# Kernel optimization log

Measured on AMD Instinct MI355X. Metric: run time of the kernel, lower is better.

The kernel has to match this reference:

```python
import jax, jax.numpy as jnp
import numpy as np

N_ENTITIES = 100_000
N_USERS = 50_000
N_HOPS = 3
R0, R1 = 42033, 44630  # hard-coded region slice in the source (2597 regions)
CHANNEL = 128
N_EDGES = 2_000_000
NNZ = 1_000_000
N_REL_ROWS = 25  # n_relations - 1


def setup_inputs() -> dict:
    key = jax.random.key(0)
    ks = jax.random.split(key, 10)
    user_emb = jax.random.normal(ks[0], (N_USERS, CHANNEL), jnp.float32) * 0.1
    entity_emb = jax.random.normal(ks[1], (N_ENTITIES, CHANNEL), jnp.float32) * 0.1
    edge_head = jax.random.randint(ks[2], (N_EDGES,), 0, N_ENTITIES, dtype=jnp.int32)
    edge_tail = jax.random.randint(ks[3], (N_EDGES,), 0, N_ENTITIES, dtype=jnp.int32)
    # edge_type in [1, n_relations-1] because weight is indexed with edge_type - 1
    edge_type = jax.random.randint(ks[4], (N_EDGES,), 1, N_REL_ROWS + 1, dtype=jnp.int32)
    interact_rows = jax.random.randint(ks[5], (NNZ,), 0, N_USERS, dtype=jnp.int32)
    interact_cols = jax.random.randint(ks[6], (NNZ,), 0, N_ENTITIES, dtype=jnp.int32)
    interact_vals = jax.random.uniform(ks[7], (NNZ,), jnp.float32)
    rw = jax.random.uniform(ks[8], (R1 - R0, R1 - R0), jnp.float32)
    region_weight_matrix = rw / jnp.sum(rw, axis=1, keepdims=True)  # row-stochastic like source
    weight = jax.random.normal(ks[9], (N_REL_ROWS, CHANNEL), jnp.float32) * 0.1
    return {
        'user_emb': user_emb,
        'entity_emb': entity_emb,
        'region_weight_matrix': region_weight_matrix,
        'weight': weight,
        'interact_vals': interact_vals,
        'edge_head': edge_head,
        'edge_tail': edge_tail,
        'edge_type': edge_type,
        'interact_rows': interact_rows,
        'interact_cols': interact_cols,
    }


def _l2_normalize(x):
    # matches F.normalize(x, p=2, dim=1, eps=1e-12)
    n = jnp.linalg.norm(x, axis=1, keepdims=True)
    return x / jnp.maximum(n, 1e-12)


def reference(user_emb, entity_emb, region_weight_matrix, weight, interact_vals,
              edge_head, edge_tail, edge_type, interact_rows, interact_cols):
    entity_res, user_res = entity_emb, user_emb
    # scatter_mean denominator (edge structure is fixed across hops)
    deg = jax.ops.segment_sum(jnp.ones_like(edge_head, dtype=entity_emb.dtype),
                              edge_head, num_segments=N_ENTITIES)
    inv_deg = jnp.where(deg > 0, 1.0 / deg, 0.0)[:, None]

    for _ in range(N_HOPS):
        # region aggregate (source uses clone().detach())
        new_ev = jax.lax.stop_gradient(entity_emb)
        region = region_weight_matrix @ new_ev[R0:R1]  # [2597, C]
        new_ev = new_ev.at[R0:R1].set(region)
        entity_emb = entity_emb * 0.8 + new_ev * 0.2
        # KG aggregate: gather, relation-weighted multiply, scatter_mean by head
        rel = weight[edge_type - 1]                 # [E, C]
        neigh = entity_emb[edge_tail] * rel          # [E, C]
        entity_agg = jax.ops.segment_sum(neigh, edge_head, num_segments=N_ENTITIES) * inv_deg
        # user aggregate: sparse mm (COO) -> segment_sum over rows
        user_agg = jax.ops.segment_sum(interact_vals[:, None] * entity_emb[interact_cols],
                                       interact_rows, num_segments=N_USERS)
        # normalize + residual (mess_dropout disabled for deterministic reference)
        entity_emb = _l2_normalize(entity_agg)
        user_emb = _l2_normalize(user_agg)
        entity_res = entity_res + entity_emb
        user_res = user_res + user_emb
    return entity_res, user_res
```

## Files before the change

kernel.cpp:

```cpp
#include <hip/hip_runtime.h>
#include <stdint.h>

#define N_ENT 100000
#define N_USR 50000
#define NREG  2597
#define REG0  42033
#define CHAN  128
#define NEDGE 2000000
#define NNZI  1000000

#define BSPAN 512
#define NB_E  196
#define NB_U  98
#define BCAP  12288
#define TILE  2048
#define EPT   8
#define NWG_E ((NEDGE + TILE - 1) / TILE)
#define NWG_U ((NNZI  + TILE - 1) / TILE)

#define MT16   163
#define MPAD   (MT16 * 16)
#define KSTEPS 82
#define KPAD   (KSTEPS * 32)
#define NKC2   8
#define SPC    ((KSTEPS + NKC2 - 1) / NKC2)

typedef unsigned int uint32;
typedef unsigned short ushort16;
using bf16x8 = __attribute__((ext_vector_type(8))) short;
using f32x4  = __attribute__((ext_vector_type(4))) float;

__device__ __forceinline__ uint32 f2bf(float x) {
  uint32 b = __float_as_uint(x);
  b += 0x7FFFu + ((b >> 16) & 1u);
  return b >> 16;
}
__device__ __forceinline__ float bf_lo(uint32 u) { return __uint_as_float(u << 16); }
__device__ __forceinline__ float bf_hi(uint32 u) { return __uint_as_float(u & 0xFFFF0000u); }


__global__ __launch_bounds__(256) void k_part_e(const int* __restrict__ head,
                                                const int* __restrict__ tail,
                                                const int* __restrict__ type,
                                                int* __restrict__ cur,
                                                uint32* __restrict__ st) {
  __shared__ int lh[NB_E], lb[NB_E];
  int tid = threadIdx.x;
  for (int i = tid; i < NB_E; i += 256) lh[i] = 0;
  __syncthreads();
  int base = blockIdx.x * TILE;
  int bk[EPT], rk[EPT]; uint32 rec[EPT];
#pragma unroll
  for (int j = 0; j < EPT; ++j) {
    int idx = base + j * 256 + tid;
    bk[j] = -1;
    if (idx < NEDGE) {
      int h = head[idx];
      uint32 loc = (uint32)(h & (BSPAN - 1));
      rec[j] = (uint32)tail[idx] | ((uint32)(type[idx] - 1) << 17) | (loc << 22);
      bk[j] = h >> 9;
      rk[j] = atomicAdd(&lh[bk[j]], 1);
    }
  }
  __syncthreads();
  for (int i = tid; i < NB_E; i += 256)
    lb[i] = lh[i] ? atomicAdd(&cur[i], lh[i]) : 0;
  __syncthreads();
#pragma unroll
  for (int j = 0; j < EPT; ++j) {
    if (bk[j] >= 0) {
      int slot = lb[bk[j]] + rk[j];
      if (slot < BCAP) st[(size_t)bk[j] * BCAP + slot] = rec[j];
    }
  }
}

__global__ __launch_bounds__(256) void k_part_u(const int* __restrict__ rows,
                                                const int* __restrict__ cols,
                                                const float* __restrict__ vals,
                                                int* __restrict__ cur,
                                                uint2* __restrict__ st) {
  __shared__ int lh[NB_U], lb[NB_U];
  int tid = threadIdx.x;
  for (int i = tid; i < NB_U; i += 256) lh[i] = 0;
  __syncthreads();
  int base = blockIdx.x * TILE;
  int bk[EPT], rk[EPT]; uint2 rec[EPT];
#pragma unroll
  for (int j = 0; j < EPT; ++j) {
    int idx = base + j * 256 + tid;
    bk[j] = -1;
    if (idx < NNZI) {
      int r = rows[idx];
      uint32 loc = (uint32)(r & (BSPAN - 1));
      rec[j] = make_uint2(__float_as_uint(vals[idx]), (uint32)cols[idx] | (loc << 17));
      bk[j] = r >> 9;
      rk[j] = atomicAdd(&lh[bk[j]], 1);
    }
  }
  __syncthreads();
  for (int i = tid; i < NB_U; i += 256)
    lb[i] = lh[i] ? atomicAdd(&cur[i], lh[i]) : 0;
  __syncthreads();
#pragma unroll
  for (int j = 0; j < EPT; ++j) {
    if (bk[j] >= 0) {
      int slot = lb[bk[j]] + rk[j];
      if (slot < BCAP) st[(size_t)bk[j] * BCAP + slot] = rec[j];
    }
  }
}

__global__ void k_bexc(const int* __restrict__ cnt, int* __restrict__ base, int nb) {
  __shared__ int t[256];
  int tid = threadIdx.x;
  int x = (tid < nb) ? cnt[tid] : 0;
  t[tid] = x;
  __syncthreads();
  for (int off = 1; off < 256; off <<= 1) {
    int y = (tid >= off) ? t[tid - off] : 0;
    __syncthreads();
    t[tid] += y;
    __syncthreads();
  }
  if (tid < nb) base[tid] = t[tid] - x;
}

__global__ __launch_bounds__(512) void k_place_e(const uint32* __restrict__ st,
                                                 const int* __restrict__ bcnt,
                                                 const int* __restrict__ bbase,
                                                 int* __restrict__ rowptr,
                                                 float* __restrict__ invdeg,
                                                 int* __restrict__ pk) {
  __shared__ int hcnt[BSPAN];
  __shared__ int sx[BSPAN];
  int tid = threadIdx.x;
  int b = blockIdx.x;
  int cnt = bcnt[b]; if (cnt > BCAP) cnt = BCAP;
  int base = bbase[b];
  int h0 = b << 9;
  hcnt[tid] = 0;
  __syncthreads();
  const uint32* bst = st + (size_t)b * BCAP;
  for (int i = tid; i < cnt; i += 512)
    atomicAdd(&hcnt[(bst[i] >> 22) & (BSPAN - 1)], 1);
  __syncthreads();
  int mycnt = hcnt[tid];
  sx[tid] = mycnt;
  __syncthreads();
  for (int off = 1; off < 512; off <<= 1) {
    int y = (tid >= off) ? sx[tid - off] : 0;
    __syncthreads();
    sx[tid] += y;
    __syncthreads();
  }
  int myex = sx[tid] - mycnt;
  int gh = h0 + tid;
  if (gh <= N_ENT) rowptr[gh] = base + myex;
  if (gh < N_ENT) invdeg[gh] = mycnt ? 1.0f / (float)mycnt : 0.0f;
  __syncthreads();
  sx[tid] = base + myex;
  hcnt[tid] = 0;
  __syncthreads();
  for (int i = tid; i < cnt; i += 512) {
    uint32 r = bst[i];
    int loc = (r >> 22) & (BSPAN - 1);
    int rk = atomicAdd(&hcnt[loc], 1);
    pk[sx[loc] + rk] = (int)(r & 0x3FFFFFu);
  }
}

__global__ __launch_bounds__(512) void k_place_u(const uint2* __restrict__ st,
                                                 const int* __restrict__ bcnt,
                                                 const int* __restrict__ bbase,
                                                 int* __restrict__ rowptr,
                                                 int2* __restrict__ pk) {
  __shared__ int hcnt[BSPAN];
  __shared__ int sx[BSPAN];
  int tid = threadIdx.x;
  int b = blockIdx.x;
  int cnt = bcnt[b]; if (cnt > BCAP) cnt = BCAP;
  int base = bbase[b];
  int h0 = b << 9;
  hcnt[tid] = 0;
  __syncthreads();
  const uint2* bst = st + (size_t)b * BCAP;
  for (int i = tid; i < cnt; i += 512)
    atomicAdd(&hcnt[bst[i].y >> 17], 1);
  __syncthreads();
  int mycnt = hcnt[tid];
  sx[tid] = mycnt;
  __syncthreads();
  for (int off = 1; off < 512; off <<= 1) {
    int y = (tid >= off) ? sx[tid - off] : 0;
    __syncthreads();
    sx[tid] += y;
    __syncthreads();
  }
  int myex = sx[tid] - mycnt;
  int gh = h0 + tid;
  if (gh <= N_USR) rowptr[gh] = base + myex;
  __syncthreads();
  sx[tid] = base + myex;
  hcnt[tid] = 0;
  __syncthreads();
  for (int i = tid; i < cnt; i += 512) {
    uint2 r = bst[i];
    int loc = r.y >> 17;
    int rk = atomicAdd(&hcnt[loc], 1);
    pk[sx[loc] + rk] = make_int2((int)(r.y & 0x1FFFFu), (int)r.x);
  }
}

__global__ void k_cast_bf16(const float* __restrict__ src, uint32* __restrict__ dst, int n4) {
  int i = blockIdx.x * blockDim.x + threadIdx.x;
  if (i < n4) {
    float4 v = *(const float4*)(src + (size_t)i * 4);
    uint32 lo = f2bf(v.x) | (f2bf(v.y) << 16);
    uint32 hi = f2bf(v.z) | (f2bf(v.w) << 16);
    *(uint2*)(dst + (size_t)i * 2) = make_uint2(lo, hi);
  }
}

__global__ void k_cast_rwb(const float* __restrict__ RW, uint32* __restrict__ RWb) {
  int i = blockIdx.x * blockDim.x + threadIdx.x;
  if (i >= MPAD * (KPAD / 8)) return;
  int r = i / (KPAD / 8);
  int k0 = (i % (KPAD / 8)) * 8;
  uint32 o[4];
  if (r < NREG) {
    const float* s = RW + (size_t)r * NREG;
#pragma unroll
    for (int j = 0; j < 4; ++j) {
      int ka = k0 + 2 * j, kb = ka + 1;
      float va = (ka < NREG) ? s[ka] : 0.f;
      float vb = (kb < NREG) ? s[kb] : 0.f;
      o[j] = f2bf(va) | (f2bf(vb) << 16);
    }
  } else {
    o[0] = o[1] = o[2] = o[3] = 0u;
  }
  *(uint4*)(RWb + (size_t)r * (KPAD / 2) + k0 / 2) = make_uint4(o[0], o[1], o[2], o[3]);
}

__global__ void k_build_rbt(const float* __restrict__ Rf, uint32* __restrict__ RbT) {
  int i = blockIdx.x * blockDim.x + threadIdx.x;
  if (i >= CHAN * (KPAD / 8)) return;
  int c = i / (KPAD / 8);
  int k0 = (i % (KPAD / 8)) * 8;
  uint32 o[4];
#pragma unroll
  for (int j = 0; j < 4; ++j) {
    int ka = k0 + 2 * j, kb = ka + 1;
    float va = (ka < NREG) ? Rf[(size_t)ka * CHAN + c] : 0.f;
    float vb = (kb < NREG) ? Rf[(size_t)kb * CHAN + c] : 0.f;
    o[j] = f2bf(va) | (f2bf(vb) << 16);
  }
  *(uint4*)(RbT + (size_t)c * (KPAD / 2) + k0 / 2) = make_uint4(o[0], o[1], o[2], o[3]);
}

__global__ __launch_bounds__(256) void k_region_mfma(const ushort16* __restrict__ RWb,
                                                     const ushort16* __restrict__ RbT,
                                                     float* __restrict__ Rtmp) {
  int lane = threadIdx.x & 63;
  int wid  = threadIdx.x >> 6;
  int mt = blockIdx.x % MT16;
  int kc = blockIdx.x / MT16;
  int m0 = mt * 16;
  int rc  = lane & 15;
  int kq  = lane >> 4;

  int s0 = kc * SPC;
  int s1 = s0 + SPC; if (s1 > KSTEPS) s1 = KSTEPS;

  f32x4 acc0 = {0.f, 0.f, 0.f, 0.f};
  f32x4 acc1 = {0.f, 0.f, 0.f, 0.f};

  const ushort16* arow = RWb + (size_t)(m0 + rc) * KPAD;
  const ushort16* b0   = RbT + (size_t)(wid * 32 + rc) * KPAD;
  const ushort16* b1   = b0 + (size_t)16 * KPAD;

  for (int s = s0; s < s1; ++s) {
    int k = s * 32 + kq * 8;
    bf16x8 a  = *(const bf16x8*)(arow + k);
    bf16x8 v0 = *(const bf16x8*)(b0 + k);
    bf16x8 v1 = *(const bf16x8*)(b1 + k);
    acc0 = __builtin_amdgcn_mfma_f32_16x16x32_bf16(a, v0, acc0, 0, 0, 0);
    acc1 = __builtin_amdgcn_mfma_f32_16x16x32_bf16(a, v1, acc1, 0, 0, 0);
  }

  int orow = m0 + kq * 4;
#pragma unroll
  for (int r = 0; r < 4; ++r) {
    int gr = orow + r;
    if (gr < NREG) {
      atomicAdd(&Rtmp[(size_t)gr * CHAN + wid * 32 + rc],      acc0[r]);
      atomicAdd(&Rtmp[(size_t)gr * CHAN + wid * 32 + 16 + rc], acc1[r]);
    }
  }
}

__global__ void k_region_apply(float* __restrict__ Rf, const float* __restrict__ Rtmp,
                               ushort16* __restrict__ curB) {
  int i = blockIdx.x * blockDim.x + threadIdx.x;
  if (i < NREG * CHAN) {
    float v = Rf[i] * 0.8f + Rtmp[i] * 0.2f;
    Rf[i] = v;
    curB[(size_t)REG0 * CHAN + i] = (ushort16)f2bf(v);
  }
}


__global__ void k_ent_agg(const ushort16* __restrict__ curB, const int* __restrict__ rowptr,
                          const int* __restrict__ pk, const float* __restrict__ Wt,
                          const float* __restrict__ invdeg,
                          uint32* __restrict__ nxtB, float* __restrict__ nxtRf,
                          float* __restrict__ out_e) {
  int gid  = blockIdx.x * blockDim.x + threadIdx.x;
  int wave = gid >> 6;
  int lane = threadIdx.x & 63;
  if (wave >= N_ENT) return;
  int h = wave;
  int beg = rowptr[h], end = rowptr[h + 1];
  int deg = end - beg;
  int e = lane >> 4;
  int q = lane & 15;

  float acc[8];
#pragma unroll
  for (int k = 0; k < 8; ++k) acc[k] = 0.f;

  int pkv = 0;
  { int idx = beg + lane; if (idx < end) pkv = pk[idx]; }

  int nch = (deg + 3) >> 2;

  uint4  evA = make_uint4(0, 0, 0, 0);
  float4 waA = make_float4(0.f, 0.f, 0.f, 0.f);
  float4 wbA = make_float4(0.f, 0.f, 0.f, 0.f);
  uint32 mA = 0;

  if (nch > 0) {
    int p = __shfl(pkv, e, 64);
    mA = (e < deg) ? 0xFFFFFFFFu : 0u;
    int t = p & 0x1FFFF;
    int r = p >> 17;
    evA = *(const uint4*)((const char*)curB + ((size_t)t << 8) + (q << 4));
    const float* wr = Wt + ((size_t)r << 7) + (q << 3);
    waA = *(const float4*)wr;
    wbA = *(const float4*)(wr + 4);
  }

  for (int ci = 0; ci < nch; ++ci) {
    uint4  evB = make_uint4(0, 0, 0, 0);
    float4 waB = make_float4(0.f, 0.f, 0.f, 0.f);
    float4 wbB = make_float4(0.f, 0.f, 0.f, 0.f);
    uint32 mB = 0;
    int cn = ci + 1;
    if (cn < nch) {
      if ((cn & 15) == 0) {
        int idx = beg + cn * 4 + lane;
        pkv = (idx < end) ? pk[idx] : 0;
      }
      int p = __shfl(pkv, (cn & 15) * 4 + e, 64);
      mB = (cn * 4 + e < deg) ? 0xFFFFFFFFu : 0u;
      int t = p & 0x1FFFF;
      int r = p >> 17;
      evB = *(const uint4*)((const char*)curB + ((size_t)t << 8) + (q << 4));
      const float* wr = Wt + ((size_t)r << 7) + (q << 3);
      waB = *(const float4*)wr;
      wbB = *(const float4*)(wr + 4);
    }
    uint4 ev = evA;
    ev.x &= mA; ev.y &= mA; ev.z &= mA; ev.w &= mA;
    acc[0] += bf_lo(ev.x) * waA.x;
    acc[1] += bf_hi(ev.x) * waA.y;
    acc[2] += bf_lo(ev.y) * waA.z;
    acc[3] += bf_hi(ev.y) * waA.w;
    acc[4] += bf_lo(ev.z) * wbA.x;
    acc[5] += bf_hi(ev.z) * wbA.y;
    acc[6] += bf_lo(ev.w) * wbA.z;
    acc[7] += bf_hi(ev.w) * wbA.w;
    evA = evB; waA = waB; wbA = wbB; mA = mB;
  }

#pragma unroll
  for (int k = 0; k < 8; ++k) {
    acc[k] += __shfl_xor(acc[k], 16, 64);
    acc[k] += __shfl_xor(acc[k], 32, 64);
  }
  float s = invdeg[h];
#pragma unroll
  for (int k = 0; k < 8; ++k) acc[k] *= s;
  float ss = 0.f;
#pragma unroll
  for (int k = 0; k < 8; ++k) ss += acc[k] * acc[k];
#pragma unroll
  for (int off = 8; off; off >>= 1) ss += __shfl_xor(ss, off, 64);
  float inv = 1.0f / fmaxf(sqrtf(ss), 1e-12f);
#pragma unroll
  for (int k = 0; k < 8; ++k) acc[k] *= inv;

  if (e == 0) {
    uint4 bpk;
    bpk.x = f2bf(acc[0]) | (f2bf(acc[1]) << 16);
    bpk.y = f2bf(acc[2]) | (f2bf(acc[3]) << 16);
    bpk.z = f2bf(acc[4]) | (f2bf(acc[5]) << 16);
    bpk.w = f2bf(acc[6]) | (f2bf(acc[7]) << 16);
    *(uint4*)((char*)nxtB + ((size_t)h << 8) + (q << 4)) = bpk;
    if (h >= REG0 && h < REG0 + NREG) {
      float* rp = nxtRf + ((size_t)(h - REG0) << 7) + (q << 3);
      *(float4*)rp       = make_float4(acc[0], acc[1], acc[2], acc[3]);
      *(float4*)(rp + 4) = make_float4(acc[4], acc[5], acc[6], acc[7]);
    }
    float* op = out_e + ((size_t)h << 7) + (q << 3);
    float4 o0 = *(const float4*)op;
    float4 o1 = *(const float4*)(op + 4);
    o0.x += acc[0]; o0.y += acc[1]; o0.z += acc[2]; o0.w += acc[3];
    o1.x += acc[4]; o1.y += acc[5]; o1.z += acc[6]; o1.w += acc[7];
    *(float4*)op       = o0;
    *(float4*)(op + 4) = o1;
  }
}

__global__ void k_usr_agg(const ushort16* __restrict__ curB, const int* __restrict__ rowptr,
                          const int2* __restrict__ pk, float* __restrict__ out_u) {
  int gid  = blockIdx.x * blockDim.x + threadIdx.x;
  int wave = gid >> 6;
  int lane = threadIdx.x & 63;
  if (wave >= N_USR) return;
  int u = wave;
  int beg = rowptr[u], end = rowptr[u + 1];
  int deg = end - beg;
  int e = lane >> 4;
  int q = lane & 15;

  float acc[8];
#pragma unroll
  for (int k = 0; k < 8; ++k) acc[k] = 0.f;

  int2 pkv = make_int2(0, 0);
  { int idx = beg + lane; if (idx < end) pkv = pk[idx]; }

  int nch = (deg + 3) >> 2;

  uint4 evA = make_uint4(0, 0, 0, 0);
  float vA = 0.f;

  if (nch > 0) {
    int col     = __shfl(pkv.x, e, 64);
    float vraw  = __int_as_float(__shfl(pkv.y, e, 64));
    vA = (e < deg) ? vraw : 0.f;
    evA = *(const uint4*)((const char*)curB + ((size_t)col << 8) + (q << 4));
  }

  for (int ci = 0; ci < nch; ++ci) {
    uint4 evB = make_uint4(0, 0, 0, 0);
    float vB = 0.f;
    int cn = ci + 1;
    if (cn < nch) {
      if ((cn & 15) == 0) {
        int idx = beg + cn * 4 + lane;
        pkv = (idx < end) ? pk[idx] : make_int2(0, 0);
      }
      int sl = (cn & 15) * 4 + e;
      int col    = __shfl(pkv.x, sl, 64);
      float vraw = __int_as_float(__shfl(pkv.y, sl, 64));
      vB = (cn * 4 + e < deg) ? vraw : 0.f;
      evB = *(const uint4*)((const char*)curB + ((size_t)col << 8) + (q << 4));
    }
    acc[0] += vA * bf_lo(evA.x);
    acc[1] += vA * bf_hi(evA.x);
    acc[2] += vA * bf_lo(evA.y);
    acc[3] += vA * bf_hi(evA.y);
    acc[4] += vA * bf_lo(evA.z);
    acc[5] += vA * bf_hi(evA.z);
    acc[6] += vA * bf_lo(evA.w);
    acc[7] += vA * bf_hi(evA.w);
    evA = evB; vA = vB;
  }

#pragma unroll
  for (int k = 0; k < 8; ++k) {
    acc[k] += __shfl_xor(acc[k], 16, 64);
    acc[k] += __shfl_xor(acc[k], 32, 64);
  }
  float ss = 0.f;
#pragma unroll
  for (int k = 0; k < 8; ++k) ss += acc[k] * acc[k];
#pragma unroll
  for (int off = 8; off; off >>= 1) ss += __shfl_xor(ss, off, 64);
  float inv = 1.0f / fmaxf(sqrtf(ss), 1e-12f);
#pragma unroll
  for (int k = 0; k < 8; ++k) acc[k] *= inv;

  if (e == 0) {
    float* op = out_u + ((size_t)u << 7) + (q << 3);
    float4 o0 = *(const float4*)op;
    float4 o1 = *(const float4*)(op + 4);
    o0.x += acc[0]; o0.y += acc[1]; o0.z += acc[2]; o0.w += acc[3];
    o1.x += acc[4]; o1.y += acc[5]; o1.z += acc[6]; o1.w += acc[7];
    *(float4*)op       = o0;
    *(float4*)(op + 4) = o1;
  }
}


extern "C" void kernel_launch(void* const* d_in, const int* in_sizes, int n_in,
                              void* d_out, int out_size, void* d_ws, size_t ws_size,
                              hipStream_t stream) {
  const float* user_emb   = (const float*)d_in[0];
  const float* entity_emb = (const float*)d_in[1];
  const float* RW         = (const float*)d_in[2];
  const float* weight     = (const float*)d_in[3];
  const float* ivals      = (const float*)d_in[4];
  const int*   e_head     = (const int*)d_in[5];
  const int*   e_tail     = (const int*)d_in[6];
  const int*   e_type     = (const int*)d_in[7];
  const int*   i_rows     = (const int*)d_in[8];
  const int*   i_cols     = (const int*)d_in[9];

  float* out_e = (float*)d_out;
  float* out_u = (float*)d_out + (size_t)N_ENT * CHAN;

  char* p = (char*)d_ws;
  size_t off = 0;
  auto carve = [&](size_t bytes) -> void* {
    void* r = p + off;
    off += (bytes + 255) & ~(size_t)255;
    return r;
  };
  ushort16* B16a   = (ushort16*)carve((size_t)N_ENT * CHAN * 2);
  ushort16* B16b   = (ushort16*)carve((size_t)N_ENT * CHAN * 2);
  ushort16* RWb    = (ushort16*)carve((size_t)MPAD * KPAD * 2);
  ushort16* RbT    = (ushort16*)carve((size_t)CHAN * KPAD * 2);
  float* Rfa       = (float*)carve((size_t)(KPAD) * CHAN * 4);
  float* Rfb       = (float*)carve((size_t)(KPAD) * CHAN * 4);
  float* Rtmp      = (float*)carve((size_t)NREG * CHAN * 4);
  float* inv_deg   = (float*)carve((size_t)N_ENT * 4);
  int*   e_rowptr  = (int*)carve((size_t)(N_ENT + 1) * 4);
  int*   e_packed  = (int*)carve((size_t)NEDGE * 4);
  int*   u_rowptr  = (int*)carve((size_t)(N_USR + 1) * 4);
  int2*  u_packed  = (int2*)carve((size_t)NNZI * 8);
  char*  st_raw    = (char*)carve((size_t)NB_E * BCAP * 4 > (size_t)NB_U * BCAP * 8
                                  ? (size_t)NB_E * BCAP * 4 : (size_t)NB_U * BCAP * 8);
  int*   e_bcur    = (int*)carve((size_t)NB_E * 4);
  int*   e_bbase   = (int*)carve((size_t)NB_E * 4);
  int*   u_bcur    = (int*)carve((size_t)NB_U * 4);
  int*   u_bbase   = (int*)carve((size_t)NB_U * 4);
  if (off > ws_size) return;

  hipMemsetAsync(e_bcur, 0, (size_t)NB_E * 4, stream);
  k_part_e<<<NWG_E, 256, 0, stream>>>(e_head, e_tail, e_type, e_bcur, (uint32*)st_raw);
  k_bexc<<<1, 256, 0, stream>>>(e_bcur, e_bbase, NB_E);
  k_place_e<<<NB_E, 512, 0, stream>>>((const uint32*)st_raw, e_bcur, e_bbase,
                                      e_rowptr, inv_deg, e_packed);

  hipMemsetAsync(u_bcur, 0, (size_t)NB_U * 4, stream);
  k_part_u<<<NWG_U, 256, 0, stream>>>(i_rows, i_cols, ivals, u_bcur, (uint2*)st_raw);
  k_bexc<<<1, 256, 0, stream>>>(u_bcur, u_bbase, NB_U);
  k_place_u<<<NB_U, 512, 0, stream>>>((const uint2*)st_raw, u_bcur, u_bbase,
                                      u_rowptr, u_packed);

  k_cast_rwb<<<(MPAD * (KPAD / 8) + 255) / 256, 256, 0, stream>>>(RW, (uint32*)RWb);
  k_cast_bf16<<<(N_ENT * CHAN / 4 + 255) / 256, 256, 0, stream>>>(
      entity_emb, (uint32*)B16a, N_ENT * CHAN / 4);
  hipMemsetAsync(Rfa, 0, (size_t)KPAD * CHAN * 4, stream);
  hipMemsetAsync(Rfb, 0, (size_t)KPAD * CHAN * 4, stream);
  hipMemcpyAsync(Rfa, entity_emb + (size_t)REG0 * CHAN, (size_t)NREG * CHAN * 4,
                 hipMemcpyDeviceToDevice, stream);
  hipMemcpyAsync(out_e, entity_emb, (size_t)N_ENT * CHAN * 4, hipMemcpyDeviceToDevice, stream);
  hipMemcpyAsync(out_u, user_emb, (size_t)N_USR * CHAN * 4, hipMemcpyDeviceToDevice, stream);

  for (int hop = 0; hop < 3; ++hop) {
    ushort16* curB = (hop & 1) ? B16b : B16a;
    ushort16* nxtB = (hop & 1) ? B16a : B16b;
    float*    curR = (hop & 1) ? Rfb : Rfa;
    float*    nxtR = (hop & 1) ? Rfa : Rfb;
    k_build_rbt<<<(CHAN * (KPAD / 8) + 255) / 256, 256, 0, stream>>>(curR, (uint32*)RbT);
    hipMemsetAsync(Rtmp, 0, (size_t)NREG * CHAN * 4, stream);
    k_region_mfma<<<MT16 * NKC2, 256, 0, stream>>>(RWb, RbT, Rtmp);
    k_region_apply<<<(NREG * CHAN + 255) / 256, 256, 0, stream>>>(curR, Rtmp, curB);
    k_ent_agg<<<(N_ENT * 64) / 256, 256, 0, stream>>>(curB, e_rowptr, e_packed, weight,
                                                      inv_deg, (uint32*)nxtB, nxtR, out_e);
    k_usr_agg<<<(N_USR * 64) / 256, 256, 0, stream>>>(curB, u_rowptr, u_packed, out_u);
  }
}
```

Before: 801.0 us.

## Use fixed bucket slots with padded rows, split-K partials, fused init, deeper gather pipeline

```diff
diff --git a/kernel.cpp b/kernel.cpp
--- a/kernel.cpp
+++ b/kernel.cpp
@@ -12,7 +12,9 @@
 #define BSPAN 512
 #define NB_E  196
 #define NB_U  98
-#define BCAP  12288
+#define BCAP  11264
+#define SLOT_E 12800
+#define SLOT_U 12800
 #define TILE  2048
 #define EPT   8
 #define NWG_E ((NEDGE + TILE - 1) / TILE)
@@ -111,25 +113,9 @@
   }
 }
 
-__global__ void k_bexc(const int* __restrict__ cnt, int* __restrict__ base, int nb) {
-  __shared__ int t[256];
-  int tid = threadIdx.x;
-  int x = (tid < nb) ? cnt[tid] : 0;
-  t[tid] = x;
-  __syncthreads();
-  for (int off = 1; off < 256; off <<= 1) {
-    int y = (tid >= off) ? t[tid - off] : 0;
-    __syncthreads();
-    t[tid] += y;
-    __syncthreads();
-  }
-  if (tid < nb) base[tid] = t[tid] - x;
-}
-
 __global__ __launch_bounds__(512) void k_place_e(const uint32* __restrict__ st,
                                                  const int* __restrict__ bcnt,
-                                                 const int* __restrict__ bbase,
-                                                 int* __restrict__ rowptr,
+                                                 int2* __restrict__ rp2,
                                                  float* __restrict__ invdeg,
                                                  int* __restrict__ pk) {
   __shared__ int hcnt[BSPAN];
@@ -137,7 +123,7 @@
   int tid = threadIdx.x;
   int b = blockIdx.x;
   int cnt = bcnt[b]; if (cnt > BCAP) cnt = BCAP;
-  int base = bbase[b];
+  int base = b * SLOT_E;
   int h0 = b << 9;
   hcnt[tid] = 0;
   __syncthreads();
@@ -146,7 +132,8 @@
     atomicAdd(&hcnt[(bst[i] >> 22) & (BSPAN - 1)], 1);
   __syncthreads();
   int mycnt = hcnt[tid];
-  sx[tid] = mycnt;
+  int mypad = (mycnt + 3) & ~3;
+  sx[tid] = mypad;
   __syncthreads();
   for (int off = 1; off < 512; off <<= 1) {
     int y = (tid >= off) ? sx[tid - off] : 0;
@@ -154,12 +141,14 @@
     sx[tid] += y;
     __syncthreads();
   }
-  int myex = sx[tid] - mycnt;
+  int start = base + sx[tid] - mypad;
   int gh = h0 + tid;
-  if (gh <= N_ENT) rowptr[gh] = base + myex;
-  if (gh < N_ENT) invdeg[gh] = mycnt ? 1.0f / (float)mycnt : 0.0f;
-  __syncthreads();
-  sx[tid] = base + myex;
+  if (gh < N_ENT) {
+    rp2[gh] = make_int2(start, start + mypad);
+    invdeg[gh] = mycnt ? 1.0f / (float)mycnt : 0.0f;
+  }
+  __syncthreads();
+  sx[tid] = start;
   hcnt[tid] = 0;
   __syncthreads();
   for (int i = tid; i < cnt; i += 512) {
@@ -168,19 +157,19 @@
     int rk = atomicAdd(&hcnt[loc], 1);
     pk[sx[loc] + rk] = (int)(r & 0x3FFFFFu);
   }
+  for (int j = mycnt; j < mypad; ++j) pk[start + j] = (25 << 17);
 }
 
 __global__ __launch_bounds__(512) void k_place_u(const uint2* __restrict__ st,
                                                  const int* __restrict__ bcnt,
-                                                 const int* __restrict__ bbase,
-                                                 int* __restrict__ rowptr,
+                                                 int2* __restrict__ rp2,
                                                  int2* __restrict__ pk) {
   __shared__ int hcnt[BSPAN];
   __shared__ int sx[BSPAN];
   int tid = threadIdx.x;
   int b = blockIdx.x;
   int cnt = bcnt[b]; if (cnt > BCAP) cnt = BCAP;
-  int base = bbase[b];
+  int base = b * SLOT_U;
   int h0 = b << 9;
   hcnt[tid] = 0;
   __syncthreads();
@@ -189,7 +178,8 @@
     atomicAdd(&hcnt[bst[i].y >> 17], 1);
   __syncthreads();
   int mycnt = hcnt[tid];
-  sx[tid] = mycnt;
+  int mypad = (mycnt + 3) & ~3;
+  sx[tid] = mypad;
   __syncthreads();
   for (int off = 1; off < 512; off <<= 1) {
     int y = (tid >= off) ? sx[tid - off] : 0;
@@ -197,11 +187,11 @@
     sx[tid] += y;
     __syncthreads();
   }
-  int myex = sx[tid] - mycnt;
+  int start = base + sx[tid] - mypad;
   int gh = h0 + tid;
-  if (gh <= N_USR) rowptr[gh] = base + myex;
-  __syncthreads();
-  sx[tid] = base + myex;
+  if (gh < N_USR) rp2[gh] = make_int2(start, start + mypad);
+  __syncthreads();
+  sx[tid] = start;
   hcnt[tid] = 0;
   __syncthreads();
   for (int i = tid; i < cnt; i += 512) {
@@ -210,15 +200,34 @@
     int rk = atomicAdd(&hcnt[loc], 1);
     pk[sx[loc] + rk] = make_int2((int)(r.y & 0x1FFFFu), (int)r.x);
   }
-}
-
-__global__ void k_cast_bf16(const float* __restrict__ src, uint32* __restrict__ dst, int n4) {
+  for (int j = mycnt; j < mypad; ++j) pk[start + j] = make_int2(0, 0);
+}
+
+__global__ void k_wt26(const float* __restrict__ w, float* __restrict__ wt) {
   int i = blockIdx.x * blockDim.x + threadIdx.x;
-  if (i < n4) {
-    float4 v = *(const float4*)(src + (size_t)i * 4);
-    uint32 lo = f2bf(v.x) | (f2bf(v.y) << 16);
-    uint32 hi = f2bf(v.z) | (f2bf(v.w) << 16);
-    *(uint2*)(dst + (size_t)i * 2) = make_uint2(lo, hi);
+  if (i < 26 * CHAN) wt[i] = (i < 25 * CHAN) ? w[i] : 0.f;
+}
+
+__global__ void k_init_ent(const float* __restrict__ src, uint32* __restrict__ dstB,
+                           float* __restrict__ out_e, float* __restrict__ Rf) {
+  int i = blockIdx.x * blockDim.x + threadIdx.x;
+  if (i >= N_ENT * CHAN / 8) return;
+  size_t o = (size_t)i * 8;
+  float4 v0 = *(const float4*)(src + o);
+  float4 v1 = *(const float4*)(src + o + 4);
+  uint4 b;
+  b.x = f2bf(v0.x) | (f2bf(v0.y) << 16);
+  b.y = f2bf(v0.z) | (f2bf(v0.w) << 16);
+  b.z = f2bf(v1.x) | (f2bf(v1.y) << 16);
+  b.w = f2bf(v1.z) | (f2bf(v1.w) << 16);
+  *(uint4*)(dstB + (size_t)i * 4) = b;
+  *(float4*)(out_e + o) = v0;
+  *(float4*)(out_e + o + 4) = v1;
+  int h = (int)(o >> 7);
+  if (h >= REG0 && h < REG0 + NREG) {
+    size_t ro = (((size_t)(h - REG0)) << 7) + (o & 127);
+    *(float4*)(Rf + ro) = v0;
+    *(float4*)(Rf + ro + 4) = v1;
   }
 }
 
@@ -261,7 +270,7 @@
 
 __global__ __launch_bounds__(256) void k_region_mfma(const ushort16* __restrict__ RWb,
                                                      const ushort16* __restrict__ RbT,
-                                                     float* __restrict__ Rtmp) {
+                                                     float* __restrict__ Rtmp8) {
   int lane = threadIdx.x & 63;
   int wid  = threadIdx.x >> 6;
   int mt = blockIdx.x % MT16;
@@ -289,29 +298,33 @@
     acc1 = __builtin_amdgcn_mfma_f32_16x16x32_bf16(a, v1, acc1, 0, 0, 0);
   }
 
+  float* dst = Rtmp8 + (size_t)kc * (NREG * CHAN);
   int orow = m0 + kq * 4;
 #pragma unroll
   for (int r = 0; r < 4; ++r) {
     int gr = orow + r;
     if (gr < NREG) {
-      atomicAdd(&Rtmp[(size_t)gr * CHAN + wid * 32 + rc],      acc0[r]);
-      atomicAdd(&Rtmp[(size_t)gr * CHAN + wid * 32 + 16 + rc], acc1[r]);
-    }
-  }
-}
-
-__global__ void k_region_apply(float* __restrict__ Rf, const float* __restrict__ Rtmp,
+      dst[(size_t)gr * CHAN + wid * 32 + rc]      = acc0[r];
+      dst[(size_t)gr * CHAN + wid * 32 + 16 + rc] = acc1[r];
+    }
+  }
+}
+
+__global__ void k_region_apply(float* __restrict__ Rf, const float* __restrict__ Rtmp8,
                                ushort16* __restrict__ curB) {
   int i = blockIdx.x * blockDim.x + threadIdx.x;
   if (i < NREG * CHAN) {
-    float v = Rf[i] * 0.8f + Rtmp[i] * 0.2f;
+    float t = 0.f;
+#pragma unroll
+    for (int c = 0; c < NKC2; ++c) t += Rtmp8[(size_t)c * (NREG * CHAN) + i];
+    float v = Rf[i] * 0.8f + t * 0.2f;
     Rf[i] = v;
     curB[(size_t)REG0 * CHAN + i] = (ushort16)f2bf(v);
   }
 }
 
 
-__global__ void k_ent_agg(const ushort16* __restrict__ curB, const int* __restrict__ rowptr,
+__global__ void k_ent_agg(const ushort16* __restrict__ curB, const int2* __restrict__ rp2,
                           const int* __restrict__ pk, const float* __restrict__ Wt,
                           const float* __restrict__ invdeg,
                           uint32* __restrict__ nxtB, float* __restrict__ nxtRf,
@@ -321,8 +334,9 @@
   int lane = threadIdx.x & 63;
   if (wave >= N_ENT) return;
   int h = wave;
-  int beg = rowptr[h], end = rowptr[h + 1];
-  int deg = end - beg;
+  int2 be = rp2[h];
+  int beg = be.x, end = be.y;
+  int nch = (end - beg) >> 2;
   int e = lane >> 4;
   int q = lane & 15;
 
@@ -333,56 +347,54 @@
   int pkv = 0;
   { int idx = beg + lane; if (idx < end) pkv = pk[idx]; }
 
-  int nch = (deg + 3) >> 2;
-
-  uint4  evA = make_uint4(0, 0, 0, 0);
-  float4 waA = make_float4(0.f, 0.f, 0.f, 0.f);
-  float4 wbA = make_float4(0.f, 0.f, 0.f, 0.f);
-  uint32 mA = 0;
-
-  if (nch > 0) {
-    int p = __shfl(pkv, e, 64);
-    mA = (e < deg) ? 0xFFFFFFFFu : 0u;
-    int t = p & 0x1FFFF;
-    int r = p >> 17;
-    evA = *(const uint4*)((const char*)curB + ((size_t)t << 8) + (q << 4));
-    const float* wr = Wt + ((size_t)r << 7) + (q << 3);
-    waA = *(const float4*)wr;
-    wbA = *(const float4*)(wr + 4);
-  }
-
-  for (int ci = 0; ci < nch; ++ci) {
-    uint4  evB = make_uint4(0, 0, 0, 0);
-    float4 waB = make_float4(0.f, 0.f, 0.f, 0.f);
-    float4 wbB = make_float4(0.f, 0.f, 0.f, 0.f);
-    uint32 mB = 0;
-    int cn = ci + 1;
-    if (cn < nch) {
-      if ((cn & 15) == 0) {
-        int idx = beg + cn * 4 + lane;
-        pkv = (idx < end) ? pk[idx] : 0;
-      }
-      int p = __shfl(pkv, (cn & 15) * 4 + e, 64);
-      mB = (cn * 4 + e < deg) ? 0xFFFFFFFFu : 0u;
-      int t = p & 0x1FFFF;
-      int r = p >> 17;
-      evB = *(const uint4*)((const char*)curB + ((size_t)t << 8) + (q << 4));
-      const float* wr = Wt + ((size_t)r << 7) + (q << 3);
-      waB = *(const float4*)wr;
-      wbB = *(const float4*)(wr + 4);
-    }
-    uint4 ev = evA;
-    ev.x &= mA; ev.y &= mA; ev.z &= mA; ev.w &= mA;
-    acc[0] += bf_lo(ev.x) * waA.x;
-    acc[1] += bf_hi(ev.x) * waA.y;
-    acc[2] += bf_lo(ev.y) * waA.z;
-    acc[3] += bf_hi(ev.y) * waA.w;
-    acc[4] += bf_lo(ev.z) * wbA.x;
-    acc[5] += bf_hi(ev.z) * wbA.y;
-    acc[6] += bf_lo(ev.w) * wbA.z;
-    acc[7] += bf_hi(ev.w) * wbA.w;
-    evA = evB; waA = waB; wbA = wbB; mA = mB;
-  }
+  uint4  ev0, ev1, ev2;
+  float4 wa0, wb0, wa1, wb1, wa2, wb2;
+
+#define E_ISSUE(CN, EV, WA, WB) do {                                        \
+    int _cn = (CN);                                                         \
+    if (_cn < nch) {                                                        \
+      if (_cn && ((_cn & 15) == 0)) {                                       \
+        int _idx = beg + _cn * 4 + lane;                                    \
+        pkv = (_idx < end) ? pk[_idx] : 0;                                  \
+      }                                                                     \
+      int _p = __shfl(pkv, ((_cn & 15) << 2) | e, 64);                      \
+      int _t = _p & 0x1FFFF;                                                \
+      int _r = _p >> 17;                                                    \
+      EV = *(const uint4*)((const char*)curB + ((size_t)_t << 8) + (q << 4)); \
+      const float* _wr = Wt + ((size_t)_r << 7) + (q << 3);                 \
+      WA = *(const float4*)_wr;                                             \
+      WB = *(const float4*)(_wr + 4);                                       \
+    }                                                                       \
+  } while (0)
+
+#define E_CONS(EV, WA, WB) do {            \
+    acc[0] += bf_lo(EV.x) * WA.x;          \
+    acc[1] += bf_hi(EV.x) * WA.y;          \
+    acc[2] += bf_lo(EV.y) * WA.z;          \
+    acc[3] += bf_hi(EV.y) * WA.w;          \
+    acc[4] += bf_lo(EV.z) * WB.x;          \
+    acc[5] += bf_hi(EV.z) * WB.y;          \
+    acc[6] += bf_lo(EV.w) * WB.z;          \
+    acc[7] += bf_hi(EV.w) * WB.w;          \
+  } while (0)
+
+  E_ISSUE(0, ev0, wa0, wb0);
+  E_ISSUE(1, ev1, wa1, wb1);
+  E_ISSUE(2, ev2, wa2, wb2);
+  for (int ci = 0; ci < nch; ci += 3) {
+    E_CONS(ev0, wa0, wb0);
+    E_ISSUE(ci + 3, ev0, wa0, wb0);
+    if (ci + 1 < nch) {
+      E_CONS(ev1, wa1, wb1);
+      E_ISSUE(ci + 4, ev1, wa1, wb1);
+    }
+    if (ci + 2 < nch) {
+      E_CONS(ev2, wa2, wb2);
+      E_ISSUE(ci + 5, ev2, wa2, wb2);
+    }
+  }
+#undef E_ISSUE
+#undef E_CONS
 
 #pragma unroll
   for (int k = 0; k < 8; ++k) {
@@ -423,15 +435,16 @@
   }
 }
 
-__global__ void k_usr_agg(const ushort16* __restrict__ curB, const int* __restrict__ rowptr,
+__global__ void k_usr_agg(const ushort16* __restrict__ curB, const int2* __restrict__ rp2,
                           const int2* __restrict__ pk, float* __restrict__ out_u) {
   int gid  = blockIdx.x * blockDim.x + threadIdx.x;
   int wave = gid >> 6;
   int lane = threadIdx.x & 63;
   if (wave >= N_USR) return;
   int u = wave;
-  int beg = rowptr[u], end = rowptr[u + 1];
-  int deg = end - beg;
+  int2 be = rp2[u];
+  int beg = be.x, end = be.y;
+  int nch = (end - beg) >> 2;
   int e = lane >> 4;
   int q = lane & 15;
 
@@ -442,43 +455,51 @@
   int2 pkv = make_int2(0, 0);
   { int idx = beg + lane; if (idx < end) pkv = pk[idx]; }
 
-  int nch = (deg + 3) >> 2;
-
-  uint4 evA = make_uint4(0, 0, 0, 0);
-  float vA = 0.f;
-
-  if (nch > 0) {
-    int col     = __shfl(pkv.x, e, 64);
-    float vraw  = __int_as_float(__shfl(pkv.y, e, 64));
-    vA = (e < deg) ? vraw : 0.f;
-    evA = *(const uint4*)((const char*)curB + ((size_t)col << 8) + (q << 4));
-  }
-
-  for (int ci = 0; ci < nch; ++ci) {
-    uint4 evB = make_uint4(0, 0, 0, 0);
-    float vB = 0.f;
-    int cn = ci + 1;
-    if (cn < nch) {
-      if ((cn & 15) == 0) {
-        int idx = beg + cn * 4 + lane;
-        pkv = (idx < end) ? pk[idx] : make_int2(0, 0);
-      }
-      int sl = (cn & 15) * 4 + e;
-      int col    = __shfl(pkv.x, sl, 64);
-      float vraw = __int_as_float(__shfl(pkv.y, sl, 64));
-      vB = (cn * 4 + e < deg) ? vraw : 0.f;
-      evB = *(const uint4*)((const char*)curB + ((size_t)col << 8) + (q << 4));
-    }
-    acc[0] += vA * bf_lo(evA.x);
-    acc[1] += vA * bf_hi(evA.x);
-    acc[2] += vA * bf_lo(evA.y);
-    acc[3] += vA * bf_hi(evA.y);
-    acc[4] += vA * bf_lo(evA.z);
-    acc[5] += vA * bf_hi(evA.z);
-    acc[6] += vA * bf_lo(evA.w);
-    acc[7] += vA * bf_hi(evA.w);
-    evA = evB; vA = vB;
-  }
+  uint4 ev0, ev1, ev2;
+  float v0, v1, v2;
+
+#define U_ISSUE(CN, EV, V) do {                                             \
+    int _cn = (CN);                                                         \
+    if (_cn < nch) {                                                        \
+      if (_cn && ((_cn & 15) == 0)) {                                       \
+        int _idx = beg + _cn * 4 + lane;                                    \
+        pkv = (_idx < end) ? pk[_idx] : make_int2(0, 0);                    \
+      }                                                                     \
+      int _sl = ((_cn & 15) << 2) | e;                                      \
+      int _c = __shfl(pkv.x, _sl, 64);                                      \
+      V = __int_as_float(__shfl(pkv.y, _sl, 64));                           \
+      EV = *(const uint4*)((const char*)curB + ((size_t)_c << 8) + (q << 4)); \
+    }                                                                       \
+  } while (0)
+
+#define U_CONS(EV, V) do {          \
+    acc[0] += V * bf_lo(EV.x);      \
+    acc[1] += V * bf_hi(EV.x);      \
+    acc[2] += V * bf_lo(EV.y);      \
+    acc[3] += V * bf_hi(EV.y);      \
+    acc[4] += V * bf_lo(EV.z);      \
+    acc[5] += V * bf_hi(EV.z);      \
+    acc[6] += V * bf_lo(EV.w);      \
+    acc[7] += V * bf_hi(EV.w);      \
+  } while (0)
+
+  U_ISSUE(0, ev0, v0);
+  U_ISSUE(1, ev1, v1);
+  U_ISSUE(2, ev2, v2);
+  for (int ci = 0; ci < nch; ci += 3) {
+    U_CONS(ev0, v0);
+    U_ISSUE(ci + 3, ev0, v0);
+    if (ci + 1 < nch) {
+      U_CONS(ev1, v1);
+      U_ISSUE(ci + 4, ev1, v1);
+    }
+    if (ci + 2 < nch) {
+      U_CONS(ev2, v2);
+      U_ISSUE(ci + 5, ev2, v2);
+    }
+  }
+#undef U_ISSUE
+#undef U_CONS
 
 #pragma unroll
   for (int k = 0; k < 8; ++k) {
@@ -534,42 +555,37 @@
   ushort16* B16b   = (ushort16*)carve((size_t)N_ENT * CHAN * 2);
   ushort16* RWb    = (ushort16*)carve((size_t)MPAD * KPAD * 2);
   ushort16* RbT    = (ushort16*)carve((size_t)CHAN * KPAD * 2);
-  float* Rfa       = (float*)carve((size_t)(KPAD) * CHAN * 4);
-  float* Rfb       = (float*)carve((size_t)(KPAD) * CHAN * 4);
-  float* Rtmp      = (float*)carve((size_t)NREG * CHAN * 4);
+  float* Rfa       = (float*)carve((size_t)NREG * CHAN * 4);
+  float* Rfb       = (float*)carve((size_t)NREG * CHAN * 4);
   float* inv_deg   = (float*)carve((size_t)N_ENT * 4);
-  int*   e_rowptr  = (int*)carve((size_t)(N_ENT + 1) * 4);
-  int*   e_packed  = (int*)carve((size_t)NEDGE * 4);
-  int*   u_rowptr  = (int*)carve((size_t)(N_USR + 1) * 4);
-  int2*  u_packed  = (int2*)carve((size_t)NNZI * 8);
-  char*  st_raw    = (char*)carve((size_t)NB_E * BCAP * 4 > (size_t)NB_U * BCAP * 8
-                                  ? (size_t)NB_E * BCAP * 4 : (size_t)NB_U * BCAP * 8);
+  float* wt26      = (float*)carve((size_t)26 * CHAN * 4);
+  int2*  e_rp2     = (int2*)carve((size_t)N_ENT * 8);
+  int*   e_packed  = (int*)carve((size_t)NB_E * SLOT_E * 4);
+  int2*  u_rp2     = (int2*)carve((size_t)N_USR * 8);
+  int2*  u_packed  = (int2*)carve((size_t)NB_U * SLOT_U * 8);
+  size_t st_bytes   = (size_t)NB_E * BCAP * 4 > (size_t)NB_U * BCAP * 8
+                      ? (size_t)NB_E * BCAP * 4 : (size_t)NB_U * BCAP * 8;
+  size_t rtmp_bytes = (size_t)NKC2 * NREG * CHAN * 4;
+  char*  shared_rg = (char*)carve(st_bytes > rtmp_bytes ? st_bytes : rtmp_bytes);
+  float* Rtmp8     = (float*)shared_rg;
   int*   e_bcur    = (int*)carve((size_t)NB_E * 4);
-  int*   e_bbase   = (int*)carve((size_t)NB_E * 4);
   int*   u_bcur    = (int*)carve((size_t)NB_U * 4);
-  int*   u_bbase   = (int*)carve((size_t)NB_U * 4);
   if (off > ws_size) return;
 
   hipMemsetAsync(e_bcur, 0, (size_t)NB_E * 4, stream);
-  k_part_e<<<NWG_E, 256, 0, stream>>>(e_head, e_tail, e_type, e_bcur, (uint32*)st_raw);
-  k_bexc<<<1, 256, 0, stream>>>(e_bcur, e_bbase, NB_E);
-  k_place_e<<<NB_E, 512, 0, stream>>>((const uint32*)st_raw, e_bcur, e_bbase,
-                                      e_rowptr, inv_deg, e_packed);
+  k_part_e<<<NWG_E, 256, 0, stream>>>(e_head, e_tail, e_type, e_bcur, (uint32*)shared_rg);
+  k_place_e<<<NB_E, 512, 0, stream>>>((const uint32*)shared_rg, e_bcur,
+                                      e_rp2, inv_deg, e_packed);
 
   hipMemsetAsync(u_bcur, 0, (size_t)NB_U * 4, stream);
-  k_part_u<<<NWG_U, 256, 0, stream>>>(i_rows, i_cols, ivals, u_bcur, (uint2*)st_raw);
-  k_bexc<<<1, 256, 0, stream>>>(u_bcur, u_bbase, NB_U);
-  k_place_u<<<NB_U, 512, 0, stream>>>((const uint2*)st_raw, u_bcur, u_bbase,
-                                      u_rowptr, u_packed);
+  k_part_u<<<NWG_U, 256, 0, stream>>>(i_rows, i_cols, ivals, u_bcur, (uint2*)shared_rg);
+  k_place_u<<<NB_U, 512, 0, stream>>>((const uint2*)shared_rg, u_bcur,
+                                      u_rp2, u_packed);
 
   k_cast_rwb<<<(MPAD * (KPAD / 8) + 255) / 256, 256, 0, stream>>>(RW, (uint32*)RWb);
-  k_cast_bf16<<<(N_ENT * CHAN / 4 + 255) / 256, 256, 0, stream>>>(
-      entity_emb, (uint32*)B16a, N_ENT * CHAN / 4);
-  hipMemsetAsync(Rfa, 0, (size_t)KPAD * CHAN * 4, stream);
-  hipMemsetAsync(Rfb, 0, (size_t)KPAD * CHAN * 4, stream);
-  hipMemcpyAsync(Rfa, entity_emb + (size_t)REG0 * CHAN, (size_t)NREG * CHAN * 4,
-                 hipMemcpyDeviceToDevice, stream);
-  hipMemcpyAsync(out_e, entity_emb, (size_t)N_ENT * CHAN * 4, hipMemcpyDeviceToDevice, stream);
+  k_wt26<<<(26 * CHAN + 255) / 256, 256, 0, stream>>>(weight, wt26);
+  k_init_ent<<<(N_ENT * CHAN / 8 + 255) / 256, 256, 0, stream>>>(
+      entity_emb, (uint32*)B16a, out_e, Rfa);
   hipMemcpyAsync(out_u, user_emb, (size_t)N_USR * CHAN * 4, hipMemcpyDeviceToDevice, stream);
 
   for (int hop = 0; hop < 3; ++hop) {
@@ -578,11 +594,10 @@
     float*    curR = (hop & 1) ? Rfb : Rfa;
     float*    nxtR = (hop & 1) ? Rfa : Rfb;
     k_build_rbt<<<(CHAN * (KPAD / 8) + 255) / 256, 256, 0, stream>>>(curR, (uint32*)RbT);
-    hipMemsetAsync(Rtmp, 0, (size_t)NREG * CHAN * 4, stream);
-    k_region_mfma<<<MT16 * NKC2, 256, 0, stream>>>(RWb, RbT, Rtmp);
-    k_region_apply<<<(NREG * CHAN + 255) / 256, 256, 0, stream>>>(curR, Rtmp, curB);
-    k_ent_agg<<<(N_ENT * 64) / 256, 256, 0, stream>>>(curB, e_rowptr, e_packed, weight,
+    k_region_mfma<<<MT16 * NKC2, 256, 0, stream>>>(RWb, RbT, Rtmp8);
+    k_region_apply<<<(NREG * CHAN + 255) / 256, 256, 0, stream>>>(curR, Rtmp8, curB);
+    k_ent_agg<<<(N_ENT * 64) / 256, 256, 0, stream>>>(curB, e_rp2, e_packed, wt26,
                                                       inv_deg, (uint32*)nxtB, nxtR, out_e);
-    k_usr_agg<<<(N_USR * 64) / 256, 256, 0, stream>>>(curB, u_rowptr, u_packed, out_u);
-  }
-}
+    k_usr_agg<<<(N_USR * 64) / 256, 256, 0, stream>>>(curB, u_rp2, u_packed, out_u);
+  }
+}
```

Result: no change. 808.6 us (+1.0%).
